# Performance work log

Measured on AMD Instinct MI355X. Metric: run time of the kernel, lower is better.

## Reference

```python
import jax, jax.numpy as jnp
import numpy as np
from jax import lax


def _conv2d(x, w, b, stride):
    # x: [B,C,H,W], w: [O,I,kh,kw], b: [O]
    y = lax.conv_general_dilated(
        x, w, window_strides=(stride, stride), padding='VALID',
        dimension_numbers=('NCHW', 'OIHW', 'NCHW'))
    return y + b[None, :, None, None]


def setup_inputs() -> dict:
    key = jax.random.key(0)
    ks = jax.random.split(key, 4)
    B, C, H, W = 8, 128, 128, 128
    x = jax.random.normal(ks[0], (B, C, H, W), dtype=jnp.float32)
    # conv weights, scaled like torch default init (~1/sqrt(fan_in))
    Wq = jax.random.normal(ks[1], (C, C, 2, 2), dtype=jnp.float32) / np.sqrt(C * 4)
    Wk = jax.random.normal(ks[2], (C, C, 2, 2), dtype=jnp.float32) / np.sqrt(C * 4)
    Wv = jax.random.normal(ks[3], (C, C, 1, 1), dtype=jnp.float32) / np.sqrt(C)
    bq = jnp.zeros((C,), dtype=jnp.float32)
    bk = jnp.zeros((C,), dtype=jnp.float32)
    bv = jnp.zeros((C,), dtype=jnp.float32)
    return {'x': x, 'Wq': Wq, 'bq': bq, 'Wk': Wk, 'bk': bk, 'Wv': Wv, 'bv': bv}


def reference(x, Wq, bq, Wk, bk, Wv, bv):
    B, C, H, W = x.shape
    # query/key: 2x2 stride-2 convs -> [B, C, (H//2)*(W//2)]
    q = _conv2d(x, Wq, bq, 2).reshape(B, C, -1)
    k = _conv2d(x, Wk, bk, 2).reshape(B, C, -1)
    # value: 1x1 conv -> [B, C, H*W]
    v = _conv2d(x, Wv, bv, 1).reshape(B, C, -1)
    # energy: [B, C, C]
    energy = jnp.einsum('bcn,bdn->bcd', q, k)
    # max-subtract trick: softmax over (row_max - energy)
    energy_new = jnp.max(energy, axis=-1, keepdims=True) - energy
    attention = jax.nn.softmax(energy_new, axis=-1)
    out = jnp.einsum('bcd,bdn->bcn', attention, v)
    return out.reshape(B, C, H, W)
```

## Files before the change

### kernel.cpp

```cpp
#include <hip/hip_runtime.h>
#include <math.h>


typedef float f32x4 __attribute__((ext_vector_type(4)));
typedef short s16x8 __attribute__((ext_vector_type(8)));

__device__ __forceinline__ unsigned short f2bf(float f) {
  union { float f; unsigned u; } v; v.f = f;
  unsigned r = v.u + 0x7FFFu + ((v.u >> 16) & 1u);
  return (unsigned short)(r >> 16);
}
__device__ __forceinline__ float bf2f(unsigned short h) {
  union { unsigned u; float f; } v; v.u = ((unsigned)h) << 16;
  return v.f;
}
__device__ __forceinline__ unsigned pack2(unsigned short a, unsigned short b) {
  return (unsigned)a | ((unsigned)b << 16);
}

__device__ __forceinline__ void stage_pair(unsigned short* Bh, unsigned short* Bl,
                                           int nl, int kloc, float4 v) {
  unsigned short hx = f2bf(v.x), hy = f2bf(v.y), hz = f2bf(v.z), hw = f2bf(v.w);
  unsigned short lx = f2bf(v.x - bf2f(hx)), ly = f2bf(v.y - bf2f(hy));
  unsigned short lz = f2bf(v.z - bf2f(hz)), lw = f2bf(v.w - bf2f(hw));
  *(unsigned*)&Bh[nl * 40 + kloc]       = pack2(hx, hy);
  *(unsigned*)&Bh[(nl + 1) * 40 + kloc] = pack2(hz, hw);
  *(unsigned*)&Bl[nl * 40 + kloc]       = pack2(lx, ly);
  *(unsigned*)&Bl[(nl + 1) * 40 + kloc] = pack2(lz, lw);
}

__global__ __launch_bounds__(256) void k_prep(
    const float* __restrict__ Wq, const float* __restrict__ Wk,
    unsigned short* __restrict__ Wth, unsigned short* __restrict__ Wtl) {
  const int f = (blockIdx.x * 256 + threadIdx.x) * 4;
  const int row = f >> 9;
  const int k   = f & 511;
  const float* src = (row < 128) ? &Wq[row * 512 + k] : &Wk[(row - 128) * 512 + k];
  float4 v = *(const float4*)src;
  unsigned short h0 = f2bf(v.x), h1 = f2bf(v.y), h2 = f2bf(v.z), h3 = f2bf(v.w);
  unsigned short l0 = f2bf(v.x - bf2f(h0)), l1 = f2bf(v.y - bf2f(h1));
  unsigned short l2 = f2bf(v.z - bf2f(h2)), l3 = f2bf(v.w - bf2f(h3));
  const int di = (k >> 5) * 8192 + row * 32 + (k & 31);
  *(ushort4*)&Wth[di] = make_ushort4(h0, h1, h2, h3);
  *(ushort4*)&Wtl[di] = make_ushort4(l0, l1, l2, l3);
}

__global__ __launch_bounds__(256, 2) void k_conv_energy(
    const float* __restrict__ x,
    const unsigned short* __restrict__ Wth, const unsigned short* __restrict__ Wtl,
    const float* __restrict__ bq, const float* __restrict__ bk,
    float* __restrict__ epart) {
  __shared__ unsigned short LDS[32768];
  unsigned short* Ah = LDS;
  unsigned short* Al = LDS + 10240;
  unsigned short* Bh = LDS + 20480;
  unsigned short* Bl = LDS + 23040;
  unsigned short* Th = LDS;
  unsigned short* Tl = LDS + 16384;

  const int t = threadIdx.x;
  const int nt = blockIdx.x, b = blockIdx.y;
  const int w = t >> 6, lane = t & 63;
  const int lrow = lane & 15, lkb = lane >> 4;

  const int pp = t >> 4;
  const int ci_l = pp >> 1, kh = pp & 1;
  const int c0 = (t & 15) * 8;
  const int klb = ci_l * 4 + kh * 2;
  const float* xb = x + ((size_t)b << 21);

  f32x4 acc[4][4];
#pragma unroll
  for (int m = 0; m < 4; ++m)
#pragma unroll
    for (int n = 0; n < 4; ++n) acc[m][n] = (f32x4){0.f, 0.f, 0.f, 0.f};

  for (int step = 0; step < 16; ++step) {
    const uint4* gh = (const uint4*)(Wth + step * 8192);
    const uint4* gl = (const uint4*)(Wtl + step * 8192);
#pragma unroll
    for (int j = 0; j < 4; ++j) {
      const int c = t + 256 * j;
      const int row = c >> 2, ko = (c & 3) * 8;
      *(uint4*)&Ah[row * 40 + ko] = gh[c];
      *(uint4*)&Al[row * 40 + ko] = gl[c];
    }
    {
      const float* xr = xb + (size_t)(step * 8 + ci_l) * 16384 + (2 * nt + kh) * 128 + c0;
      float4 v1 = *(const float4*)&xr[0];
      float4 v2 = *(const float4*)&xr[4];
      stage_pair(Bh, Bl, c0 >> 1, klb, v1);
      stage_pair(Bh, Bl, (c0 >> 1) + 2, klb, v2);
    }
    __syncthreads();
    s16x8 afh[4], afl[4], bfh[4], bfl[4];
#pragma unroll
    for (int m = 0; m < 4; ++m) {
      const int aidx = (w * 64 + m * 16 + lrow) * 40 + lkb * 8;
      afh[m] = *(const s16x8*)&Ah[aidx];
      afl[m] = *(const s16x8*)&Al[aidx];
    }
#pragma unroll
    for (int n = 0; n < 4; ++n) {
      const int bidx = (n * 16 + lrow) * 40 + lkb * 8;
      bfh[n] = *(const s16x8*)&Bh[bidx];
      bfl[n] = *(const s16x8*)&Bl[bidx];
    }
#pragma unroll
    for (int m = 0; m < 4; ++m)
#pragma unroll
      for (int n = 0; n < 4; ++n) {
        acc[m][n] = __builtin_amdgcn_mfma_f32_16x16x32_bf16(afh[m], bfh[n], acc[m][n], 0, 0, 0);
        acc[m][n] = __builtin_amdgcn_mfma_f32_16x16x32_bf16(afh[m], bfl[n], acc[m][n], 0, 0, 0);
        acc[m][n] = __builtin_amdgcn_mfma_f32_16x16x32_bf16(afl[m], bfh[n], acc[m][n], 0, 0, 0);
      }
    __syncthreads();
  }

#pragma unroll
  for (int m = 0; m < 4; ++m) {
    const int r0 = w * 64 + m * 16 + (lane >> 4) * 4;
#pragma unroll
    for (int n = 0; n < 4; ++n) {
      const int c = n * 16 + lrow;
      const int c8 = c >> 3, c7 = c & 7;
#pragma unroll
      for (int i = 0; i < 4; ++i) {
        const int r = r0 + i;
        const float bias = (r < 128) ? bq[r] : bk[r - 128];
        const float vv = acc[m][n][i] + bias;
        const unsigned short h = f2bf(vv);
        const unsigned short l = f2bf(vv - bf2f(h));
        const int ad = r * 64 + (((c8 ^ (r & 7))) << 3) + c7;
        Th[ad] = h;
        Tl[ad] = l;
      }
    }
  }
  __syncthreads();

  f32x4 e[4][4];
#pragma unroll
  for (int m = 0; m < 4; ++m)
#pragma unroll
    for (int n = 0; n < 4; ++n) e[m][n] = (f32x4){0.f, 0.f, 0.f, 0.f};

  const int mrow0 = (w >> 1) * 64;
  const int nrow0 = 128 + (w & 1) * 64;
#pragma unroll
  for (int ks = 0; ks < 2; ++ks) {
    const int c8 = ks * 4 + lkb;
    s16x8 qh[4], ql[4], kh8[4], kl8[4];
#pragma unroll
    for (int m = 0; m < 4; ++m) {
      const int r = mrow0 + m * 16 + lrow;
      const int ad = r * 64 + ((c8 ^ (r & 7)) << 3);
      qh[m] = *(const s16x8*)&Th[ad];
      ql[m] = *(const s16x8*)&Tl[ad];
    }
#pragma unroll
    for (int n = 0; n < 4; ++n) {
      const int r = nrow0 + n * 16 + lrow;
      const int ad = r * 64 + ((c8 ^ (r & 7)) << 3);
      kh8[n] = *(const s16x8*)&Th[ad];
      kl8[n] = *(const s16x8*)&Tl[ad];
    }
#pragma unroll
    for (int m = 0; m < 4; ++m)
#pragma unroll
      for (int n = 0; n < 4; ++n) {
        e[m][n] = __builtin_amdgcn_mfma_f32_16x16x32_bf16(qh[m], kh8[n], e[m][n], 0, 0, 0);
        e[m][n] = __builtin_amdgcn_mfma_f32_16x16x32_bf16(qh[m], kl8[n], e[m][n], 0, 0, 0);
        e[m][n] = __builtin_amdgcn_mfma_f32_16x16x32_bf16(ql[m], kh8[n], e[m][n], 0, 0, 0);
      }
  }
  float* ep = epart + ((size_t)b * 64 + nt) * 16384;
#pragma unroll
  for (int m = 0; m < 4; ++m) {
    const int qr = (w >> 1) * 64 + m * 16 + (lane >> 4) * 4;
#pragma unroll
    for (int n = 0; n < 4; ++n) {
      const int kr = (w & 1) * 64 + n * 16 + lrow;
#pragma unroll
      for (int i = 0; i < 4; ++i) ep[(size_t)(qr + i) * 128 + kr] = e[m][n][i];
    }
  }
}

__global__ __launch_bounds__(256) void k_softmax_M(
    const float* __restrict__ epart, const float* __restrict__ Wv,
    const float* __restrict__ bv, float* __restrict__ Mbuf,
    float* __restrict__ outbb) {
  __shared__ float As[4][128];
  const int t = threadIdx.x;
  const int wid = t >> 6, lane = t & 63;
  const int b = blockIdx.x >> 5;
  const int c = (blockIdx.x & 31) * 4 + wid;
  const int d0 = lane * 2;

  float2 s = make_float2(0.f, 0.f);
#pragma unroll 4
  for (int p = 0; p < 64; ++p) {
    float2 e = *(const float2*)&epart[((size_t)b * 64 + p) * 16384 + c * 128 + d0];
    s.x += e.x; s.y += e.y;
  }
  float mn = fminf(s.x, s.y);
#pragma unroll
  for (int off = 1; off < 64; off <<= 1) mn = fminf(mn, __shfl_xor(mn, off));
  const float p0 = expf(mn - s.x);
  const float p1 = expf(mn - s.y);
  float tot = p0 + p1;
#pragma unroll
  for (int off = 1; off < 64; off <<= 1) tot += __shfl_xor(tot, off);
  const float inv = 1.f / tot;
  const float a0 = p0 * inv, a1 = p1 * inv;

  const float2 bvv = *(const float2*)&bv[d0];
  float ob = a0 * bvv.x + a1 * bvv.y;
#pragma unroll
  for (int off = 1; off < 64; off <<= 1) ob += __shfl_xor(ob, off);
  if (lane == 0) outbb[b * 128 + c] = ob;

  As[wid][d0] = a0;
  As[wid][d0 + 1] = a1;
  float m0 = 0.f, m1 = 0.f;
#pragma unroll 4
  for (int d = 0; d < 128; ++d) {
    const float a = As[wid][d];
    const float2 wv = *(const float2*)&Wv[d * 128 + d0];
    m0 = fmaf(a, wv.x, m0);
    m1 = fmaf(a, wv.y, m1);
  }
  *(float2*)&Mbuf[(size_t)b * 16384 + c * 128 + d0] = make_float2(m0, m1);
}

__global__ __launch_bounds__(256) void k_out(
    const float* __restrict__ x, const float* __restrict__ Mbuf,
    const float* __restrict__ outbb, float* __restrict__ out) {
  __shared__ unsigned short Ms[128 * 40];
  __shared__ unsigned short Xs[128 * 40];
  const int t = threadIdx.x;
  const int nt = blockIdx.x, b = blockIdx.y;
  const int wid = t >> 6, lane = t & 63;
  const int wr = wid >> 1, wc = wid & 1;
  const int lrow = lane & 15, lkb = lane >> 4;
  const int am = t >> 1, ak0 = (t & 1) * 16;
  const int xkl = (t >> 5) * 4;
  const int xc0 = (t & 31) * 4;

  const float* xb = x + ((size_t)b << 21);
  const float* Mb = Mbuf + (size_t)b * 16384;
  float* ob = out + ((size_t)b << 21);

  f32x4 acc[4][4];
#pragma unroll
  for (int m = 0; m < 4; ++m)
#pragma unroll
    for (int n = 0; n < 4; ++n) acc[m][n] = (f32x4){0.f, 0.f, 0.f, 0.f};

  for (int step = 0; step < 4; ++step) {
    const int kk = step * 32;
    {
      float w[16];
      *(float4*)&w[0]  = *(const float4*)&Mb[am * 128 + kk + ak0];
      *(float4*)&w[4]  = *(const float4*)&Mb[am * 128 + kk + ak0 + 4];
      *(float4*)&w[8]  = *(const float4*)&Mb[am * 128 + kk + ak0 + 8];
      *(float4*)&w[12] = *(const float4*)&Mb[am * 128 + kk + ak0 + 12];
      unsigned short hs[16];
#pragma unroll
      for (int i = 0; i < 16; ++i) hs[i] = f2bf(w[i]);
      *(uint4*)&Ms[am * 40 + ak0]     = *(uint4*)&hs[0];
      *(uint4*)&Ms[am * 40 + ak0 + 8] = *(uint4*)&hs[8];
    }
#pragma unroll
    for (int q = 0; q < 4; ++q) {
      const int kl = xkl + q;
      float4 v = *(const float4*)&xb[(size_t)(kk + kl) * 16384 + nt * 128 + xc0];
      Xs[(xc0 + 0) * 40 + kl] = f2bf(v.x);
      Xs[(xc0 + 1) * 40 + kl] = f2bf(v.y);
      Xs[(xc0 + 2) * 40 + kl] = f2bf(v.z);
      Xs[(xc0 + 3) * 40 + kl] = f2bf(v.w);
    }
    __syncthreads();
    s16x8 af[4], bf[4];
#pragma unroll
    for (int m = 0; m < 4; ++m)
      af[m] = *(const s16x8*)&Ms[(wr * 64 + m * 16 + lrow) * 40 + lkb * 8];
#pragma unroll
    for (int n = 0; n < 4; ++n)
      bf[n] = *(const s16x8*)&Xs[(wc * 64 + n * 16 + lrow) * 40 + lkb * 8];
#pragma unroll
    for (int m = 0; m < 4; ++m)
#pragma unroll
      for (int n = 0; n < 4; ++n)
        acc[m][n] = __builtin_amdgcn_mfma_f32_16x16x32_bf16(af[m], bf[n], acc[m][n], 0, 0, 0);
    __syncthreads();
  }
#pragma unroll
  for (int m = 0; m < 4; ++m) {
    const int r0 = wr * 64 + m * 16 + (lane >> 4) * 4;
#pragma unroll
    for (int n = 0; n < 4; ++n) {
      const int gc = nt * 128 + wc * 64 + n * 16 + (lane & 15);
#pragma unroll
      for (int i = 0; i < 4; ++i) {
        const int row = r0 + i;
        ob[(size_t)row * 16384 + gc] = acc[m][n][i] + outbb[b * 128 + row];
      }
    }
  }
}

extern "C" void kernel_launch(void* const* d_in, const int* in_sizes, int n_in,
                              void* d_out, int out_size, void* d_ws, size_t ws_size,
                              hipStream_t stream) {
  const float* x  = (const float*)d_in[0];
  const float* Wq = (const float*)d_in[1];
  const float* bq = (const float*)d_in[2];
  const float* Wk = (const float*)d_in[3];
  const float* bk = (const float*)d_in[4];
  const float* Wv = (const float*)d_in[5];
  const float* bv = (const float*)d_in[6];
  float* out = (float*)d_out;
  char* ws = (char*)d_ws;

  float* epart = (float*)ws;
  float* Mbuf  = (float*)(ws + 33554432);
  float* outbb = (float*)(ws + 34078720);
  unsigned short* Wth = (unsigned short*)(ws + 34082816);
  unsigned short* Wtl = (unsigned short*)(ws + 34344960);

  hipLaunchKernelGGL(k_prep, dim3(128), dim3(256), 0, stream, Wq, Wk, Wth, Wtl);
  hipLaunchKernelGGL(k_conv_energy, dim3(64, 8), dim3(256), 0, stream,
                     x, Wth, Wtl, bq, bk, epart);
  hipLaunchKernelGGL(k_softmax_M, dim3(256), dim3(256), 0, stream,
                     epart, Wv, bv, Mbuf, outbb);
  hipLaunchKernelGGL(k_out, dim3(128, 8), dim3(256), 0, stream,
                     x, Mbuf, outbb, out);
}
```

Before: 93.96 us.

## Prefetch next conv-energy K-step into registers and swizzle B tile staging

The conv+energy GEMM loop now loads the next step's weight and input slices from global memory into registers right after the barrier, so the loads overlap the MFMA work of the current step. The B-operand staging is remapped so each thread handles one input channel across two kernel rows, with an XOR swizzle on the LDS column group to reduce bank conflicts on writes and fragment reads. Bias values are hoisted into registers before the epilogue. This raises register pressure under the two-blocks-per-SM launch bound and could cause spills.

```diff
diff --git a/kernel.cpp b/kernel.cpp
--- a/kernel.cpp
+++ b/kernel.cpp
@@ -13,20 +13,6 @@
 __device__ __forceinline__ float bf2f(unsigned short h) {
   union { unsigned u; float f; } v; v.u = ((unsigned)h) << 16;
   return v.f;
-}
-__device__ __forceinline__ unsigned pack2(unsigned short a, unsigned short b) {
-  return (unsigned)a | ((unsigned)b << 16);
-}
-
-__device__ __forceinline__ void stage_pair(unsigned short* Bh, unsigned short* Bl,
-                                           int nl, int kloc, float4 v) {
-  unsigned short hx = f2bf(v.x), hy = f2bf(v.y), hz = f2bf(v.z), hw = f2bf(v.w);
-  unsigned short lx = f2bf(v.x - bf2f(hx)), ly = f2bf(v.y - bf2f(hy));
-  unsigned short lz = f2bf(v.z - bf2f(hz)), lw = f2bf(v.w - bf2f(hw));
-  *(unsigned*)&Bh[nl * 40 + kloc]       = pack2(hx, hy);
-  *(unsigned*)&Bh[(nl + 1) * 40 + kloc] = pack2(hz, hw);
-  *(unsigned*)&Bl[nl * 40 + kloc]       = pack2(lx, ly);
-  *(unsigned*)&Bl[(nl + 1) * 40 + kloc] = pack2(lz, lw);
 }
 
 __global__ __launch_bounds__(256) void k_prep(
@@ -63,10 +49,12 @@
   const int w = t >> 6, lane = t & 63;
   const int lrow = lane & 15, lkb = lane >> 4;
 
-  const int pp = t >> 4;
-  const int ci_l = pp >> 1, kh = pp & 1;
-  const int c0 = (t & 15) * 8;
-  const int klb = ci_l * 4 + kh * 2;
+  const int ci_ = t >> 5;
+  const int c0 = (t & 31) * 4;
+  const int n0 = c0 >> 1;
+  const int gB = ci_ >> 1;
+  const int halfB = (ci_ & 1) * 4;
+  const int gsB = gB ^ ((n0 >> 2) & 3);
   const float* xb = x + ((size_t)b << 21);
 
   f32x4 acc[4][4];
@@ -75,24 +63,56 @@
 #pragma unroll
     for (int n = 0; n < 4; ++n) acc[m][n] = (f32x4){0.f, 0.f, 0.f, 0.f};
 
+  uint4 pah[4], pal[4];
+  float4 pb0, pb1;
+  {
+    const uint4* gh = (const uint4*)Wth;
+    const uint4* gl = (const uint4*)Wtl;
+#pragma unroll
+    for (int j = 0; j < 4; ++j) { pah[j] = gh[t + 256 * j]; pal[j] = gl[t + 256 * j]; }
+    const float* xr = xb + (size_t)ci_ * 16384 + (2 * nt) * 128 + c0;
+    pb0 = *(const float4*)xr;
+    pb1 = *(const float4*)(xr + 128);
+  }
+
   for (int step = 0; step < 16; ++step) {
-    const uint4* gh = (const uint4*)(Wth + step * 8192);
-    const uint4* gl = (const uint4*)(Wtl + step * 8192);
 #pragma unroll
     for (int j = 0; j < 4; ++j) {
       const int c = t + 256 * j;
       const int row = c >> 2, ko = (c & 3) * 8;
-      *(uint4*)&Ah[row * 40 + ko] = gh[c];
-      *(uint4*)&Al[row * 40 + ko] = gl[c];
+      *(uint4*)&Ah[row * 40 + ko] = pah[j];
+      *(uint4*)&Al[row * 40 + ko] = pal[j];
     }
     {
-      const float* xr = xb + (size_t)(step * 8 + ci_l) * 16384 + (2 * nt + kh) * 128 + c0;
-      float4 v1 = *(const float4*)&xr[0];
-      float4 v2 = *(const float4*)&xr[4];
-      stage_pair(Bh, Bl, c0 >> 1, klb, v1);
-      stage_pair(Bh, Bl, (c0 >> 1) + 2, klb, v2);
+      const float e0[4] = {pb0.x, pb0.y, pb1.x, pb1.y};
+      const float e1[4] = {pb0.z, pb0.w, pb1.z, pb1.w};
+      ushort4 h0, l0, h1, l1;
+#pragma unroll
+      for (int i = 0; i < 4; ++i) {
+        const unsigned short a = f2bf(e0[i]);
+        ((unsigned short*)&h0)[i] = a;
+        ((unsigned short*)&l0)[i] = f2bf(e0[i] - bf2f(a));
+        const unsigned short bshort = f2bf(e1[i]);
+        ((unsigned short*)&h1)[i] = bshort;
+        ((unsigned short*)&l1)[i] = f2bf(e1[i] - bf2f(bshort));
+      }
+      const int a0 = n0 * 40 + gsB * 8 + halfB;
+      const int a1 = (n0 + 1) * 40 + gsB * 8 + halfB;
+      *(ushort4*)&Bh[a0] = h0;
+      *(ushort4*)&Bl[a0] = l0;
+      *(ushort4*)&Bh[a1] = h1;
+      *(ushort4*)&Bl[a1] = l1;
     }
     __syncthreads();
+    if (step < 15) {
+      const uint4* gh = (const uint4*)(Wth + (step + 1) * 8192);
+      const uint4* gl = (const uint4*)(Wtl + (step + 1) * 8192);
+#pragma unroll
+      for (int j = 0; j < 4; ++j) { pah[j] = gh[t + 256 * j]; pal[j] = gl[t + 256 * j]; }
+      const float* xr = xb + (size_t)((step + 1) * 8 + ci_) * 16384 + (2 * nt) * 128 + c0;
+      pb0 = *(const float4*)xr;
+      pb1 = *(const float4*)(xr + 128);
+    }
     s16x8 afh[4], afl[4], bfh[4], bfl[4];
 #pragma unroll
     for (int m = 0; m < 4; ++m) {
@@ -101,10 +121,11 @@
       afl[m] = *(const s16x8*)&Al[aidx];
     }
 #pragma unroll
-    for (int n = 0; n < 4; ++n) {
-      const int bidx = (n * 16 + lrow) * 40 + lkb * 8;
-      bfh[n] = *(const s16x8*)&Bh[bidx];
-      bfl[n] = *(const s16x8*)&Bl[bidx];
+    for (int nf = 0; nf < 4; ++nf) {
+      const int row = nf * 16 + lrow;
+      const int bidx = row * 40 + (lkb ^ ((row >> 2) & 3)) * 8;
+      bfh[nf] = *(const s16x8*)&Bh[bidx];
+      bfl[nf] = *(const s16x8*)&Bl[bidx];
     }
 #pragma unroll
     for (int m = 0; m < 4; ++m)
@@ -117,6 +138,15 @@
     __syncthreads();
   }
 
+  const float* biasp = (w < 2) ? bq : bk;
+  const int rb = (w & 1) * 64;
+  float biasr[16];
+#pragma unroll
+  for (int m = 0; m < 4; ++m)
+#pragma unroll
+    for (int i = 0; i < 4; ++i)
+      biasr[m * 4 + i] = biasp[rb + m * 16 + (lane >> 4) * 4 + i];
+
 #pragma unroll
   for (int m = 0; m < 4; ++m) {
     const int r0 = w * 64 + m * 16 + (lane >> 4) * 4;
@@ -127,8 +157,7 @@
 #pragma unroll
       for (int i = 0; i < 4; ++i) {
         const int r = r0 + i;
-        const float bias = (r < 128) ? bq[r] : bk[r - 128];
-        const float vv = acc[m][n][i] + bias;
+        const float vv = acc[m][n][i] + biasr[m * 4 + i];
         const unsigned short h = f2bf(vv);
         const unsigned short l = f2bf(vv - bf2f(h));
         const int ad = r * 64 + (((c8 ^ (r & 7))) << 3) + c7;
```

New measurement: 121.4 us. 29.3% more time.

## Double-buffer x tile in LDS and read weight fragments directly from global

Applied to the files above, without the earlier changes.

The conv-energy main loop now prefetches the next x slice into registers while the MFMAs for the current step run, then stages it into an alternate LDS buffer, so each step needs one barrier instead of two. Weight A-fragments are loaded straight from global memory (pre-transposed layout) rather than staged through LDS, which frees LDS and drops the cooperative copy. Bias values are hoisted into registers before the epilogue. The trade-off is that weight reads now depend on L2/L1 latency inside the loop, plus extra register pressure from the prefetch.

```diff
diff --git a/kernel.cpp b/kernel.cpp
--- a/kernel.cpp
+++ b/kernel.cpp
@@ -51,10 +51,6 @@
     const float* __restrict__ bq, const float* __restrict__ bk,
     float* __restrict__ epart) {
   __shared__ unsigned short LDS[32768];
-  unsigned short* Ah = LDS;
-  unsigned short* Al = LDS + 10240;
-  unsigned short* Bh = LDS + 20480;
-  unsigned short* Bl = LDS + 23040;
   unsigned short* Th = LDS;
   unsigned short* Tl = LDS + 16384;
 
@@ -68,6 +64,7 @@
   const int c0 = (t & 15) * 8;
   const int klb = ci_l * 4 + kh * 2;
   const float* xb = x + ((size_t)b << 21);
+  const float* xrow = xb + (size_t)ci_l * 16384 + (2 * nt + kh) * 128 + c0;
 
   f32x4 acc[4][4];
 #pragma unroll
@@ -75,36 +72,40 @@
 #pragma unroll
     for (int n = 0; n < 4; ++n) acc[m][n] = (f32x4){0.f, 0.f, 0.f, 0.f};
 
+  {
+    float4 v1 = *(const float4*)&xrow[0];
+    float4 v2 = *(const float4*)&xrow[4];
+    stage_pair(LDS, LDS + 2560, c0 >> 1, klb, v1);
+    stage_pair(LDS, LDS + 2560, (c0 >> 1) + 2, klb, v2);
+  }
+  __syncthreads();
+
+  int cur = 0;
   for (int step = 0; step < 16; ++step) {
-    const uint4* gh = (const uint4*)(Wth + step * 8192);
-    const uint4* gl = (const uint4*)(Wtl + step * 8192);
-#pragma unroll
-    for (int j = 0; j < 4; ++j) {
-      const int c = t + 256 * j;
-      const int row = c >> 2, ko = (c & 3) * 8;
-      *(uint4*)&Ah[row * 40 + ko] = gh[c];
-      *(uint4*)&Al[row * 40 + ko] = gl[c];
-    }
+    float4 pv1, pv2;
+    if (step < 15) {
+      const float* xr = xrow + (size_t)(step + 1) * 8 * 16384;
+      pv1 = *(const float4*)&xr[0];
+      pv2 = *(const float4*)&xr[4];
+    }
+    s16x8 afh[4], afl[4], bfh[4], bfl[4];
     {
-      const float* xr = xb + (size_t)(step * 8 + ci_l) * 16384 + (2 * nt + kh) * 128 + c0;
-      float4 v1 = *(const float4*)&xr[0];
-      float4 v2 = *(const float4*)&xr[4];
-      stage_pair(Bh, Bl, c0 >> 1, klb, v1);
-      stage_pair(Bh, Bl, (c0 >> 1) + 2, klb, v2);
-    }
-    __syncthreads();
-    s16x8 afh[4], afl[4], bfh[4], bfl[4];
-#pragma unroll
-    for (int m = 0; m < 4; ++m) {
-      const int aidx = (w * 64 + m * 16 + lrow) * 40 + lkb * 8;
-      afh[m] = *(const s16x8*)&Ah[aidx];
-      afl[m] = *(const s16x8*)&Al[aidx];
-    }
-#pragma unroll
-    for (int n = 0; n < 4; ++n) {
-      const int bidx = (n * 16 + lrow) * 40 + lkb * 8;
-      bfh[n] = *(const s16x8*)&Bh[bidx];
-      bfl[n] = *(const s16x8*)&Bl[bidx];
+      const unsigned short* Wh_s = Wth + step * 8192;
+      const unsigned short* Wl_s = Wtl + step * 8192;
+#pragma unroll
+      for (int m = 0; m < 4; ++m) {
+        const int off = (w * 64 + m * 16 + lrow) * 32 + lkb * 8;
+        afh[m] = *(const s16x8*)&Wh_s[off];
+        afl[m] = *(const s16x8*)&Wl_s[off];
+      }
+    }
+    const unsigned short* Bh = LDS + cur * 5120;
+    const unsigned short* Bl = Bh + 2560;
+#pragma unroll
+    for (int nf = 0; nf < 4; ++nf) {
+      const int bidx = (nf * 16 + lrow) * 40 + lkb * 8;
+      bfh[nf] = *(const s16x8*)&Bh[bidx];
+      bfl[nf] = *(const s16x8*)&Bl[bidx];
     }
 #pragma unroll
     for (int m = 0; m < 4; ++m)
@@ -114,8 +115,24 @@
         acc[m][n] = __builtin_amdgcn_mfma_f32_16x16x32_bf16(afh[m], bfl[n], acc[m][n], 0, 0, 0);
         acc[m][n] = __builtin_amdgcn_mfma_f32_16x16x32_bf16(afl[m], bfh[n], acc[m][n], 0, 0, 0);
       }
+    if (step < 15) {
+      unsigned short* Nh = LDS + (cur ^ 1) * 5120;
+      unsigned short* Nl = Nh + 2560;
+      stage_pair(Nh, Nl, c0 >> 1, klb, pv1);
+      stage_pair(Nh, Nl, (c0 >> 1) + 2, klb, pv2);
+    }
     __syncthreads();
-  }
+    cur ^= 1;
+  }
+
+  const float* biasp = (w < 2) ? bq : bk;
+  const int rb = (w & 1) * 64;
+  float biasr[16];
+#pragma unroll
+  for (int m = 0; m < 4; ++m)
+#pragma unroll
+    for (int i = 0; i < 4; ++i)
+      biasr[m * 4 + i] = biasp[rb + m * 16 + (lane >> 4) * 4 + i];
 
 #pragma unroll
   for (int m = 0; m < 4; ++m) {
@@ -127,8 +144,7 @@
 #pragma unroll
       for (int i = 0; i < 4; ++i) {
         const int r = r0 + i;
-        const float bias = (r < 128) ? bq[r] : bk[r - 128];
-        const float vv = acc[m][n][i] + bias;
+        const float vv = acc[m][n][i] + biasr[m * 4 + i];
         const unsigned short h = f2bf(vv);
         const unsigned short l = f2bf(vv - bf2f(h));
         const int ad = r * 64 + (((c8 ^ (r & 7))) << 3) + c7;
```

Result: faster. 87.62 us (-6.7%).
